# Kernel optimization log

Hardware: AMD Instinct MI355X
Metric: run time of the kernel (lower is better)

Reference implementation:

```python
import jax, jax.numpy as jnp
import numpy as np
from jax import lax

C_LIGHT = 3e8
SPATIAL, CROP = 64, 128
BIN_LEN, WALL, SAMP_COEFF, CYCLES = 0.01, 2.0, 2.0, 5
B, D = 2, 1


def _waveconvparam(bin_resolution, virtual_wavelength, cycles):
    samples = int(round(cycles * virtual_wavelength / (C_LIGHT * bin_resolution)))
    num_cycles = samples * (C_LIGHT * bin_resolution) / virtual_wavelength
    sigma = 0.3
    g = np.arange(samples, dtype=np.float64)
    env = np.exp(-(((g - samples / 2.0) / (samples / 2.0)) ** 2) / (2 * sigma ** 2))
    cos_k = np.cos(2 * np.pi * num_cycles * g / samples) * env
    sin_k = np.sin(2 * np.pi * num_cycles * g / samples) * env
    return cos_k, sin_k


def _define_psf(N, M, slope):
    # LCT psf: locus of min |(4 slope)^2 (x^2+y^2) - z|, normalized and circularly shifted
    x = np.arange(2 * N, dtype=np.float64) / (2 * N - 1) * 2 - 1
    z = np.arange(2 * M, dtype=np.float64) / (2 * M - 1) * 2
    gy, gx, gz = np.meshgrid(x, x, z)  # (2N,2N,2M)
    blur = np.abs((4 * slope) ** 2 * (gx ** 2 + gy ** 2) - gz)
    d = (np.abs(blur - blur.min(axis=2, keepdims=True)) < 1e-8).astype(np.float64)
    e = d / np.sqrt(d.sum())
    f = np.roll(np.roll(e, N, axis=0), N, axis=1)
    return np.transpose(f, (2, 0, 1))  # (2M,2N,2N)


def _resampling_operator(M):
    row = M * M
    x = np.arange(1, row + 1, dtype=np.float64)
    mtx = np.zeros((row, M), dtype=np.float64)
    mtx[np.arange(row), np.ceil(np.sqrt(x)).astype(np.int64) - 1] = 1.0
    mtx = mtx / np.sqrt(x)[:, None]
    mtxi = mtx.T.copy()
    for _ in range(int(np.log2(M))):
        mtx = 0.5 * (mtx[0::2] + mtx[1::2])
        mtxi = 0.5 * (mtxi[:, 0::2] + mtxi[:, 1::2])
    return mtx.astype(np.float32), mtxi.astype(np.float32)


def setup_inputs() -> dict:
    key = jax.random.key(0)
    kf, kw, kb = jax.random.split(key, 3)
    bin_res = BIN_LEN / C_LIGHT
    trange = CROP * C_LIGHT * bin_res
    slope = (WALL / 2.0) / trange
    vlam = SAMP_COEFF * 2.0 * (WALL / (SPATIAL - 1))
    cos_k, sin_k = _waveconvparam(bin_res, vlam, CYCLES)
    wave = np.stack([cos_k, sin_k], 0)[:, ::-1][:, None, :].astype(np.float32)  # (2,1,k)
    psf = _define_psf(SPATIAL, CROP, slope)
    invpsf = np.conj(np.fft.fftn(psf))
    mtx, mtxi = _resampling_operator(CROP)
    return {
        "feature": jax.random.normal(kf, (B, D, CROP, SPATIAL, SPATIAL), jnp.float32),
        "conv_w": jax.random.normal(kw, ()) * 0.1 + 1.0,
        "conv_b": jax.random.normal(kb, ()) * 0.1,
        "wave": jnp.asarray(wave),
        "invpsf_real": jnp.asarray(np.real(invpsf).astype(np.float32))[None],
        "invpsf_imag": jnp.asarray(np.imag(invpsf).astype(np.float32))[None],
        "mtx": jnp.asarray(mtx),
        "mtxi": jnp.asarray(mtxi),
    }


def _attention(k1, k2, w, b):
    # SE-style cross attention; Conv3d(1,1,1) on unbatched (C=1,T,H,W) is w*x+b
    T = k2.shape[1]
    pe = jnp.sin(jnp.arange(T, dtype=k2.dtype))  # PE3D with 1 channel -> sin along T
    k2p = k2 + pe[None, :, None, None]
    scal = jnp.mean(w * k1 + b)  # conv + adaptive_avg_pool3d(1), channel dim = 1
    q = (w * k2p + b).reshape(1, 1, -1)
    attn = jax.nn.sigmoid(jax.nn.softmax(scal * q, axis=2)).reshape(k2p.shape)
    return attn * k2p


def _fre_atten2(kernel, w, b):
    _, T, H, W = kernel.shape
    ct, ch, cw = T // 2, H // 2, W // 2
    st, sh, sw = (T - ct) // 2, (H - ch) // 2, (W - cw) // 2
    sl = (slice(None), slice(ct - st, ct + st), slice(ch - sh, ch + sh), slice(cw - sw, cw + sw))
    high = kernel[sl]
    low = jnp.roll(kernel, (ct, ch, cw), axis=(1, 2, 3))[sl]
    l2l = _attention(low, low, w, b)
    l2h = _attention(l2l, high, w, b)
    temp = kernel.at[sl].set(l2h)
    temp = jnp.roll(temp, (ct, ch, cw), axis=(1, 2, 3)).at[sl].set(l2l)
    return jnp.roll(temp, (ct, ch, cw), axis=(1, 2, 3))


def _forward(feature, conv_w, conv_b, wave, invpsf_real, invpsf_imag, mtx, mtxi):
    b, d, T, H, W = feature.shape
    BD = b * d
    k = wave.shape[2]
    # virtual wave conv along time: (BDHW,1,T) x (2,1,k)
    data = feature.reshape(BD, T, H, W).transpose(0, 2, 3, 1).reshape(-1, 1, T)
    conv = lax.conv_general_dilated(data, wave, (1,), [(k // 2, k // 2)],
                                    dimension_numbers=("NCH", "OIH", "NCH"))
    if k % 2 == 0:
        conv = conv[:, :, 1:]
    data2 = conv.reshape(BD, H, W, 2, T).transpose(3, 0, 4, 1, 2).reshape(2 * BD, T, H, W)
    # temporal resampling then zero-pad to 2T,2H,2W
    tmp = jnp.einsum("tm,bmx->btx", mtx, data2.reshape(2 * BD, T, H * W)).reshape(2 * BD, T, H, W)
    datapad = jnp.zeros((2 * BD, 2 * T, 2 * H, 2 * W), feature.dtype).at[:, :T, :H, :W].set(tmp)
    datafre = jnp.fft.fftn(datapad)  # torch.fft.fftn transforms ALL dims incl. batch
    w1 = _fre_atten2(invpsf_real, conv_w, conv_b)
    w2 = _fre_atten2(invpsf_imag, conv_w, conv_b)
    re_real = datafre.real * w1 - datafre.imag * w2
    re_imag = datafre.real * w2 + datafre.imag * w1
    re = jnp.fft.ifftn(lax.complex(re_real, re_imag))
    vol = re[:, :T, :H, :W]
    cr, ci = vol[:BD].real, vol[:BD].imag
    sr, si = vol[BD:].real, vol[BD:].imag
    sum_real = cr ** 2 - ci ** 2 + sr ** 2 - si ** 2
    sum_imag = 2 * cr * ci + 2 * sr * si
    mag = jax.nn.relu((jnp.sqrt(sum_real ** 2 + sum_imag ** 2) + sum_real) * 0.5)
    sq = jnp.sqrt(mag)
    out = jnp.einsum("tm,bmx->btx", mtxi, sq.reshape(BD, T, H * W))
    return out.reshape(b, d, T, H, W)


def reference(feature, conv_w, conv_b, wave, invpsf_real, invpsf_imag, mtx, mtxi):
    return _forward(feature, conv_w, conv_b, wave, invpsf_real, invpsf_imag, mtx, mtxi)
```

## Files before the change

kernel.cpp:

```cpp
#include <hip/hip_runtime.h>

#define BLKE 524288
#define VOLE 4194304
#define TCROP 2097152
#define PI2 6.283185307179586476925286766559

__device__ __forceinline__ float2 cmulf(float2 a, float2 b){
  return make_float2(a.x*b.x - a.y*b.y, a.x*b.y + a.y*b.x);
}
__device__ __forceinline__ float waveSum(float v){
  #pragma unroll
  for (int o=32;o;o>>=1) v += __shfl_xor(v,o);
  return v;
}
__device__ __forceinline__ float waveMaxf(float v){
  #pragma unroll
  for (int o=32;o;o>>=1) v = fmaxf(v,__shfl_xor(v,o));
  return v;
}
__device__ __forceinline__ float waveMinf(float v){
  #pragma unroll
  for (int o=32;o;o>>=1) v = fminf(v,__shfl_xor(v,o));
  return v;
}

__device__ __forceinline__ void bcastReduce5(const float* __restrict__ pA, int kap,
    float& sum, float& mnl, float& mxl, float& mnh, float& mxh, float* sm ){
  int tid = threadIdx.x;
  const float* q = pA + kap*1280 + tid*5;
  float s = q[0], a = q[1], b = q[2], c = q[3], d = q[4];
  s = waveSum(s); a = waveMinf(a); b = waveMaxf(b); c = waveMinf(c); d = waveMaxf(d);
  if ((tid&63)==0){ int w = tid>>6; sm[w]=s; sm[4+w]=a; sm[8+w]=b; sm[12+w]=c; sm[16+w]=d; }
  __syncthreads();
  sum = sm[0]+sm[1]+sm[2]+sm[3];
  mnl = fminf(fminf(sm[4],sm[5]),fminf(sm[6],sm[7]));
  mxl = fmaxf(fmaxf(sm[8],sm[9]),fmaxf(sm[10],sm[11]));
  mnh = fminf(fminf(sm[12],sm[13]),fminf(sm[14],sm[15]));
  mxh = fmaxf(fmaxf(sm[16],sm[17]),fmaxf(sm[18],sm[19]));
}

__device__ __forceinline__ float bcastSum256(const float* __restrict__ p, float* sm ){
  int tid = threadIdx.x;
  float s = waveSum(p[tid]);
  if ((tid&63)==0) sm[tid>>6] = s;
  __syncthreads();
  return sm[0]+sm[1]+sm[2]+sm[3];
}

__global__ void __launch_bounds__(256) kD1(const float* __restrict__ mtx,
                                           const float* __restrict__ wave,
                                           float* __restrict__ M,
                                           const float* __restrict__ Kr,
                                           const float* __restrict__ Ki,
                                           float* __restrict__ Lw, float* __restrict__ Hw,
                                           float* __restrict__ pA,
                                           float2* __restrict__ twF,
                                           float2* __restrict__ twD,
                                           float2* __restrict__ twI){
  __shared__ float spe[128];
  __shared__ float sm[20];
  int bid = blockIdx.x;
  int tid = threadIdx.x;
  if (bid < 512){
    int kap = bid >> 8, bx = bid & 255;
    const float* K = kap ? Ki : Kr;
    if (tid < 128) spe[tid] = sinf((float)tid);
    __syncthreads();
    float sum=0.f, mnl=3.4e38f, mxl=-3.4e38f, mnh=3.4e38f, mxh=-3.4e38f;
    int base = bx*256 + tid;
    #pragma unroll
    for (int it = 0; it < 8; it++){
      int e = base + it*65536;
      int tau = e >> 12, rem = e & 4095, eta = rem >> 6, om = rem & 63;
      float pe = spe[tau];
      float lo = K[(size_t)((tau+192)&255)*16384 + ((eta+96)&127)*128 + ((om+96)&127)];
      float hi = K[(size_t)(tau+64)*16384 + (eta+32)*128 + (om+32)];
      sum += lo;
      float lp = lo+pe, hp = hi+pe;
      Lw[kap*BLKE + e] = lp;
      Hw[kap*BLKE + e] = hp;
      mnl=fminf(mnl,lp); mxl=fmaxf(mxl,lp);
      mnh=fminf(mnh,hp); mxh=fmaxf(mxh,hp);
    }
    sum = waveSum(sum); mnl=waveMinf(mnl); mxl=waveMaxf(mxl); mnh=waveMinf(mnh); mxh=waveMaxf(mxh);
    if ((tid&63)==0){ int w=tid>>6; sm[w]=sum; sm[4+w]=mnl; sm[8+w]=mxl; sm[12+w]=mnh; sm[16+w]=mxh; }
    __syncthreads();
    if (tid==0){
      float* o = pA + kap*1280 + bx*5;
      o[0] = sm[0]+sm[1]+sm[2]+sm[3];
      o[1] = fminf(fminf(sm[4],sm[5]),fminf(sm[6],sm[7]));
      o[2] = fmaxf(fmaxf(sm[8],sm[9]),fmaxf(sm[10],sm[11]));
      o[3] = fminf(fminf(sm[12],sm[13]),fminf(sm[14],sm[15]));
      o[4] = fmaxf(fmaxf(sm[16],sm[17]),fmaxf(sm[18],sm[19]));
    }
  } else if (bid < 640){
    int idx = (bid-512)*256 + tid;
    int o = idx >> 14, r = idx & 16383;
    int t = r >> 7, s = r & 127;
    float acc = 0.f;
    int mlo = s-31; if (mlo < 0) mlo = 0;
    int mhi = s+31; if (mhi > 127) mhi = 127;
    for (int m = mlo; m <= mhi; m++) acc += mtx[t*128+m]*wave[o*63 + (s-m+31)];
    M[idx] = acc;
  } else {
    if (tid < 256){
      double ang = -PI2 * (double)tid / 256.0;
      twF[tid] = make_float2((float)cos(ang), (float)sin(ang));
    }
    if (tid < 64){
      double a2 = -PI2 * (double)tid / 128.0;
      twD[tid] = make_float2((float)cos(a2), (float)sin(a2));
      double a3 =  PI2 * (double)tid / 128.0;
      twI[tid] = make_float2((float)cos(a3), (float)sin(a3));
    }
  }
}

__global__ void __launch_bounds__(256) kD2(const float* __restrict__ feat,
                                           const float* __restrict__ M,
                                           float* __restrict__ tmp,
                                           const float* __restrict__ pA,
                                           const float* __restrict__ Lw,
                                           float* __restrict__ pB,
                                           const float* cw, const float* cb){
  __shared__ __align__(16) char smem[16640];
  __shared__ float sm[20], smo[4];
  int bid = blockIdx.x;
  int tid = threadIdx.x;
  if (bid < 512){
    int kap = bid >> 8, bx = bid & 255;
    float sum,mnl,mxl,mnh,mxh;
    bcastReduce5(pA,kap,sum,mnl,mxl,mnh,mxh,sm);
    float w = cw[0], b = cb[0];
    float s1 = w*(sum*(1.0f/BLKE)) + b;
    float a1 = s1*w, c1 = s1*b;
    float mx = (a1>=0.f) ? a1*mxl+c1 : a1*mnl+c1;
    float acc = 0.f;
    int base = kap*BLKE + bx*256 + tid;
    #pragma unroll
    for (int it = 0; it < 8; it++){
      float lp = Lw[base + it*65536];
      acc += expf(a1*lp + c1 - mx);
    }
    acc = waveSum(acc);
    if ((tid&63)==0) smo[tid>>6] = acc;
    __syncthreads();
    if (tid==0) pB[kap*256 + bx] = smo[0]+smo[1]+smo[2]+smo[3];
  } else {
    int e = bid - 512;
    int b = e >> 8, tt = (e >> 6) & 3, xt = e & 63;
    float (*LF)[64] = (float(*)[64])smem;
    float (*LM)[32][33] = (float(*)[32][33])(smem + 8192);
    int xx = tid & 63, tq = tid >> 6;
    float acc0[8] = {}, acc1[8] = {};
    const float* fb = feat + (size_t)b*BLKE;
    for (int sb = 0; sb < 4; sb++){
      #pragma unroll
      for (int j = 0; j < 8; j++){
        int idx = tid + j*256; int s = idx >> 6, x = idx & 63;
        LF[s][x] = fb[(size_t)(sb*32+s)*4096 + xt*64 + x];
      }
      #pragma unroll
      for (int j = 0; j < 8; j++){
        int idx = tid + j*256; int o = idx >> 10, r = idx & 1023;
        int trow = r >> 5, s = r & 31;
        LM[o][trow][s] = M[o*16384 + (tt*32+trow)*128 + sb*32+s];
      }
      __syncthreads();
      for (int s = 0; s < 32; s++){
        float f = LF[s][xx];
        #pragma unroll
        for (int i = 0; i < 8; i++){
          acc0[i] += LM[0][tq*8+i][s]*f;
          acc1[i] += LM[1][tq*8+i][s]*f;
        }
      }
      __syncthreads();
    }
    #pragma unroll
    for (int i = 0; i < 8; i++){
      int t = tt*32 + tq*8 + i;
      tmp[(size_t)(0*2+b)*BLKE + (size_t)t*4096 + xt*64+xx] = acc0[i];
      tmp[(size_t)(1*2+b)*BLKE + (size_t)t*4096 + xt*64+xx] = acc1[i];
    }
  }
}

__global__ void __launch_bounds__(256) kD3(const float* __restrict__ tmp,
                                           float2* __restrict__ Z2,
                                           const float* __restrict__ pA,
                                           const float* __restrict__ pB,
                                           const float* __restrict__ Lw,
                                           float* __restrict__ pC,
                                           const float* cw, const float* cb,
                                           const float2* __restrict__ twg){
  __shared__ __align__(16) char smem[8832];
  __shared__ float sm[20], smB[4], smo[4];
  int bid = blockIdx.x;
  int tid = threadIdx.x;
  if (bid < 512){
    int kap = bid >> 8, bx = bid & 255;
    float sum,mnl,mxl,mnh,mxh;
    bcastReduce5(pA,kap,sum,mnl,mxl,mnh,mxh,sm);
    float d1 = bcastSum256(pB + kap*256, smB);
    float w = cw[0], b = cb[0];
    float s1 = w*(sum*(1.0f/BLKE)) + b;
    float a1 = s1*w, c1 = s1*b;
    float mx = (a1>=0.f) ? a1*mxl+c1 : a1*mnl+c1;
    float invd = 1.0f/d1;
    float acc = 0.f;
    int base = kap*BLKE + bx*256 + tid;
    #pragma unroll
    for (int it = 0; it < 8; it++){
      float lp = Lw[base + it*65536];
      float p = expf(a1*lp + c1 - mx)*invd;
      acc += lp/(1.f + expf(-p));
    }
    acc = waveSum(acc);
    if ((tid&63)==0) smo[tid>>6] = acc;
    __syncthreads();
    if (tid==0) pC[kap*256 + bx] = smo[0]+smo[1]+smo[2]+smo[3];
  } else {
    int e = bid - 512;
    int b = e >> 11, bx = e & 2047;
    float2 (*bA)[130] = (float2(*)[130])smem;
    float2 (*bB)[130] = (float2(*)[130])(smem + 4160);
    float2* tw = (float2*)(smem + 8320);
    if (tid < 64) tw[tid] = twg[tid];
    int l = tid >> 6, lane = tid & 63;
    int line = bx*4 + l;
    int t = line >> 6, h = line & 63;
    const float* pc = tmp + (size_t)b*BLKE + (size_t)t*4096 + h*64;
    const float* ps = tmp + (size_t)(2+b)*BLKE + (size_t)t*4096 + h*64;
    bA[l][lane] = make_float2(pc[lane], ps[lane]);
    bA[l][lane+64] = make_float2(0.f, 0.f);
    __syncthreads();
    float2 (*src)[130] = bA, (*dst)[130] = bB;
    int m = 1;
    #pragma unroll
    for (int st = 0; st < 7; st++){
      int i = lane;
      int jm = i & ~(m-1);
      float2 a = src[l][i], b2 = src[l][i+64];
      float2 s = make_float2(a.x+b2.x, a.y+b2.y);
      float2 d = make_float2(a.x-b2.x, a.y-b2.y);
      dst[l][i+jm]   = s;
      dst[l][i+jm+m] = cmulf(d, tw[jm]);
      __syncthreads();
      float2 (*tp)[130] = src; src = dst; dst = tp;
      m <<= 1;
    }
    float2* outp = Z2 + (size_t)b*TCROP + (size_t)t*16384 + (size_t)h*128;
    outp[lane]    = src[l][lane];
    outp[lane+64] = src[l][lane+64];
  }
}

__global__ void __launch_bounds__(256) kD4(float2* __restrict__ Z2,
                                           const float* __restrict__ pA,
                                           const float* __restrict__ pC,
                                           const float* __restrict__ Hw,
                                           float* __restrict__ pD,
                                           const float* cw, const float* cb,
                                           const float2* __restrict__ twg){
  __shared__ __align__(16) char smem[33792];
  __shared__ float sm[20], smC[4], smo[4];
  int bid = blockIdx.x;
  int tid = threadIdx.x;
  if (bid < 512){
    int kap = bid >> 8, bx = bid & 255;
    float sum,mnl,mxl,mnh,mxh;
    bcastReduce5(pA,kap,sum,mnl,mxl,mnh,mxh,sm);
    float sl2 = bcastSum256(pC + kap*256, smC);
    float w = cw[0], b = cb[0];
    float s2 = w*(sl2*(1.0f/BLKE)) + b;
    float a2 = s2*w, c2 = s2*b;
    float mx = (a2>=0.f) ? a2*mxh+c2 : a2*mnh+c2;
    float acc = 0.f;
    int base = kap*BLKE + bx*256 + tid;
    #pragma unroll
    for (int it = 0; it < 8; it++){
      float hp = Hw[base + it*65536];
      acc += expf(a2*hp + c2 - mx);
    }
    acc = waveSum(acc);
    if ((tid&63)==0) smo[tid>>6] = acc;
    __syncthreads();
    if (tid==0) pD[kap*256 + bx] = smo[0]+smo[1]+smo[2]+smo[3];
  } else {
    int e = bid - 512;
    int b = e >> 10, bx = e & 1023;
    float2 (*bA)[130] = (float2(*)[130])smem;
    float2 (*bB)[130] = (float2(*)[130])(smem + 16640);
    float2* tw = (float2*)(smem + 33280);
    if (tid < 64) tw[tid] = twg[tid];
    float2* Z = Z2 + (size_t)b*TCROP;
    int t = bx >> 3; int w0 = (bx & 7) << 4;
    size_t base = (size_t)t*16384 + w0;
    #pragma unroll
    for (int q = 0; q < 4; q++){
      int idx = q*256 + tid; int wl = idx & 15, hh = idx >> 4;
      bA[wl][hh] = Z[base + (size_t)hh*128 + wl];
      bA[wl][hh+64] = make_float2(0.f, 0.f);
    }
    __syncthreads();
    float2 (*src)[130] = bA, (*dst)[130] = bB;
    int m = 1;
    #pragma unroll
    for (int st = 0; st < 7; st++){
      #pragma unroll
      for (int q = 0; q < 4; q++){
        int g = q*256 + tid; int li = g >> 6; int i = g & 63;
        int jm = i & ~(m-1);
        float2 a = src[li][i], b2 = src[li][i+64];
        float2 s = make_float2(a.x+b2.x, a.y+b2.y);
        float2 d = make_float2(a.x-b2.x, a.y-b2.y);
        dst[li][i+jm]   = s;
        dst[li][i+jm+m] = cmulf(d, tw[jm]);
      }
      __syncthreads();
      float2 (*tp)[130] = src; src = dst; dst = tp;
      m <<= 1;
    }
    #pragma unroll
    for (int q = 0; q < 8; q++){
      int idx = q*256 + tid; int wl = idx & 15, hh = idx >> 4;
      Z[base + (size_t)hh*128 + wl] = src[wl][hh];
    }
  }
}

__device__ __forceinline__ float attnv(float v, float a, float c, float mx, float invd){
  float p = expf(a*v + c - mx)*invd;
  return v / (1.f + expf(-p));
}
__device__ __forceinline__ float2 wcAt(int t, int h, int w,
                                       const float* __restrict__ Kr, const float* __restrict__ Ki,
                                       const float* spe, const float* P){
  size_t off = (size_t)t*16384 + (size_t)h*128 + w;
  float kr = Kr[off], ki = Ki[off];
  bool center = (t>=64 && t<192) && (h>=32 && h<96) && (w>=32 && w<96);
  int tc = (t+64)&255, hc = (h+32)&127, wc = (w+32)&127;
  bool corner = (tc<128) && (hc<64) && (wc<64);
  bool act = center || corner;
  float pe = spe[(center ? (t-64) : tc) & 127];
  float A0 = center?P[4]:P[0],   C0 = center?P[5]:P[1];
  float M0 = center?P[6]:P[2],   I0 = center?P[7]:P[3];
  float A1 = center?P[12]:P[8],  C1 = center?P[13]:P[9];
  float M1 = center?P[14]:P[10], I1 = center?P[15]:P[11];
  float ox = attnv(kr+pe, A0, C0, M0, I0);
  float oy = attnv(ki+pe, A1, C1, M1, I1);
  return make_float2(act?ox:kr, act?oy:ki);
}

__global__ void __launch_bounds__(256) kP(const float* __restrict__ pA,
                                          const float* __restrict__ pB,
                                          const float* __restrict__ pC,
                                          const float* __restrict__ pD,
                                          const float* cw, const float* cb,
                                          float* __restrict__ Pg){
  __shared__ float sm[20], smB[4], smC[4], smD[4];
  int tid = threadIdx.x;
  for (int kap = 0; kap < 2; kap++){
    if (kap) __syncthreads();
    float sum,mnl,mxl,mnh,mxh;
    bcastReduce5(pA,kap,sum,mnl,mxl,mnh,mxh,sm);
    float d1  = bcastSum256(pB + kap*256, smB);
    float sl2 = bcastSum256(pC + kap*256, smC);
    float d2  = bcastSum256(pD + kap*256, smD);
    if (tid==0){
      float w = cw[0], b = cb[0];
      float s1 = w*(sum*(1.0f/BLKE)) + b;
      float a1 = s1*w, c1 = s1*b;
      float mx1 = (a1>=0.f) ? a1*mxl+c1 : a1*mnl+c1;
      float s2 = w*(sl2*(1.0f/BLKE)) + b;
      float a2 = s2*w, c2 = s2*b;
      float mx2 = (a2>=0.f) ? a2*mxh+c2 : a2*mnh+c2;
      float* Q = Pg + kap*8;
      Q[0]=a1; Q[1]=c1; Q[2]=mx1; Q[3]=1.0f/d1;
      Q[4]=a2; Q[5]=c2; Q[6]=mx2; Q[7]=1.0f/d2;
    }
  }
}

__global__ void __launch_bounds__(256) kWc(const float* __restrict__ Kr,
                                           const float* __restrict__ Ki,
                                           const float* __restrict__ Pg,
                                           float2* __restrict__ Wc){
  __shared__ float spe[128];
  __shared__ float P[16];
  int tid = threadIdx.x;
  if (tid < 128) spe[tid] = sinf((float)tid);
  else if (tid < 144) P[tid-128] = Pg[tid-128];
  __syncthreads();
  #pragma unroll
  for (int q = 0; q < 4; q++){
    int idx = blockIdx.x*1024 + q*256 + tid;
    int t = idx >> 14, r = idx & 16383, h = r >> 7, w = r & 127;
    Wc[idx] = wcAt(t, h, w, Kr, Ki, spe, P);
  }
}

__global__ void __launch_bounds__(512) kTfused(const float2* __restrict__ Z2,
                                               float2* __restrict__ U2,
                                               float2* __restrict__ V2,
                                               const float2* __restrict__ Wc,
                                               const float2* __restrict__ twg){
  __shared__ float2 buf[16][259];
  __shared__ float2 tw[256];
  int tid = threadIdx.x;
  if (tid < 256) tw[tid] = twg[tid];
  int b = blockIdx.y;
  int bid = blockIdx.x;
  int h = bid >> 3, w0 = (bid & 7) << 4;
  int wl = tid & 15, pq = tid >> 4;
  const float2* Z = Z2 + (size_t)b*TCROP;
  size_t gbase = (size_t)h*128 + w0 + wl;
  #pragma unroll
  for (int q = 0; q < 4; q++){
    int p = q*32 + pq;
    buf[wl][p] = Z[(size_t)p*16384 + gbase];
    buf[wl][p+128] = make_float2(0.f, 0.f);
  }
  __syncthreads();
  #pragma unroll
  for (int st = 0; st < 4; st++){
    const int Q = 64 >> (2*st);
    const int f = 1 << (2*st);
    #pragma unroll
    for (int it = 0; it < 2; it++){
      int u = pq + 32*it;
      int j = u & (Q-1);
      int seg = u >> (6 - 2*st);
      int base = (seg << (8 - 2*st)) + j;
      float2 a0 = buf[wl][base];
      float2 a1 = buf[wl][base+Q];
      float2 a2 = buf[wl][base+2*Q];
      float2 a3 = buf[wl][base+3*Q];
      float2 t0 = make_float2(a0.x+a2.x, a0.y+a2.y);
      float2 t1 = make_float2(a0.x-a2.x, a0.y-a2.y);
      float2 t2 = make_float2(a1.x+a3.x, a1.y+a3.y);
      float2 t3 = make_float2(a1.x-a3.x, a1.y-a3.y);
      float2 z0 = make_float2(t0.x+t2.x, t0.y+t2.y);
      float2 z2 = make_float2(t0.x-t2.x, t0.y-t2.y);
      float2 z1 = make_float2(t1.x+t3.y, t1.y-t3.x);
      float2 z3 = make_float2(t1.x-t3.y, t1.y+t3.x);
      buf[wl][base]     = z0;
      buf[wl][base+Q]   = cmulf(z1, tw[f*j]);
      buf[wl][base+2*Q] = cmulf(z2, tw[2*f*j]);
      buf[wl][base+3*Q] = cmulf(z3, tw[3*f*j]);
    }
    __syncthreads();
  }
  float2 rg[8];
  #pragma unroll
  for (int q = 0; q < 8; q++) rg[q] = buf[wl][q*32 + pq];
  #pragma unroll
  for (int q = 0; q < 8; q++){
    int p = q*32 + pq;
    int kt = ((p&3)<<6) | (((p>>2)&3)<<4) | (((p>>4)&3)<<2) | ((p>>6)&3);
    float2 wc = Wc[(size_t)kt*16384 + (size_t)h*128 + w0 + wl];
    buf[wl][p] = cmulf(rg[q], wc);
  }
  __syncthreads();
  #pragma unroll
  for (int st = 0; st < 4; st++){
    const int Q = 1 << (2*st);
    const int f = 64 >> (2*st);
    #pragma unroll
    for (int it = 0; it < 2; it++){
      int u = pq + 32*it;
      int j = u & (Q-1);
      int seg = u >> (2*st);
      int base = (seg << (2*st + 2)) + j;
      float2 w1 = tw[f*j], w2 = tw[2*f*j], w3 = tw[3*f*j];
      float2 a0 = buf[wl][base];
      float2 r1 = buf[wl][base+Q];
      float2 r2 = buf[wl][base+2*Q];
      float2 r3 = buf[wl][base+3*Q];
      float2 b1 = make_float2(r1.x*w1.x + r1.y*w1.y, r1.y*w1.x - r1.x*w1.y);
      float2 b2 = make_float2(r2.x*w2.x + r2.y*w2.y, r2.y*w2.x - r2.x*w2.y);
      float2 b3 = make_float2(r3.x*w3.x + r3.y*w3.y, r3.y*w3.x - r3.x*w3.y);
      float2 t0 = make_float2(a0.x+b2.x, a0.y+b2.y);
      float2 t1 = make_float2(a0.x-b2.x, a0.y-b2.y);
      float2 t2 = make_float2(b1.x+b3.x, b1.y+b3.y);
      float2 t3 = make_float2(b1.x-b3.x, b1.y-b3.y);
      buf[wl][base]     = make_float2(t0.x+t2.x, t0.y+t2.y);
      buf[wl][base+Q]   = make_float2(t1.x-t3.y, t1.y+t3.x);
      buf[wl][base+2*Q] = make_float2(t0.x-t2.x, t0.y-t2.y);
      buf[wl][base+3*Q] = make_float2(t1.x+t3.y, t1.y-t3.x);
    }
    __syncthreads();
  }
  float2* Uo = U2 + (size_t)b*TCROP;
  #pragma unroll
  for (int q = 0; q < 4; q++){
    int p = q*32 + pq;
    Uo[(size_t)p*16384 + gbase] = buf[wl][p];
  }
  #pragma unroll
  for (int q = 0; q < 8; q++){
    int p = q*32 + pq;
    int kt = ((p&3)<<6) | (((p>>2)&3)<<4) | (((p>>4)&3)<<2) | ((p>>6)&3);
    int tm = (256-kt)&255, hm = (128-h)&127, wm = (128-(w0+wl))&127;
    float2 wc = Wc[(size_t)tm*16384 + (size_t)hm*128 + wm];
    wc.y = -wc.y;
    buf[wl][p] = cmulf(rg[q], wc);
  }
  __syncthreads();
  #pragma unroll
  for (int st = 0; st < 4; st++){
    const int Q = 1 << (2*st);
    const int f = 64 >> (2*st);
    #pragma unroll
    for (int it = 0; it < 2; it++){
      int u = pq + 32*it;
      int j = u & (Q-1);
      int seg = u >> (2*st);
      int base = (seg << (2*st + 2)) + j;
      float2 w1 = tw[f*j], w2 = tw[2*f*j], w3 = tw[3*f*j];
      float2 a0 = buf[wl][base];
      float2 r1 = buf[wl][base+Q];
      float2 r2 = buf[wl][base+2*Q];
      float2 r3 = buf[wl][base+3*Q];
      float2 b1 = make_float2(r1.x*w1.x + r1.y*w1.y, r1.y*w1.x - r1.x*w1.y);
      float2 b2 = make_float2(r2.x*w2.x + r2.y*w2.y, r2.y*w2.x - r2.x*w2.y);
      float2 b3 = make_float2(r3.x*w3.x + r3.y*w3.y, r3.y*w3.x - r3.x*w3.y);
      float2 t0 = make_float2(a0.x+b2.x, a0.y+b2.y);
      float2 t1 = make_float2(a0.x-b2.x, a0.y-b2.y);
      float2 t2 = make_float2(b1.x+b3.x, b1.y+b3.y);
      float2 t3 = make_float2(b1.x-b3.x, b1.y-b3.y);
      buf[wl][base]     = make_float2(t0.x+t2.x, t0.y+t2.y);
      buf[wl][base+Q]   = make_float2(t1.x-t3.y, t1.y+t3.x);
      buf[wl][base+2*Q] = make_float2(t0.x-t2.x, t0.y-t2.y);
      buf[wl][base+3*Q] = make_float2(t1.x+t3.y, t1.y-t3.x);
    }
    __syncthreads();
  }
  float2* Vo = V2 + (size_t)b*TCROP;
  #pragma unroll
  for (int q = 0; q < 4; q++){
    int p = q*32 + pq;
    Vo[(size_t)p*16384 + gbase] = buf[wl][p];
  }
}

__global__ void __launch_bounds__(1024) kHW(const float2* __restrict__ U2,
                                            const float2* __restrict__ V2,
                                            float* __restrict__ sq,
                                            const float2* __restrict__ twg){
  __shared__ float2 plane[16384];
  __shared__ float2 tw[64];
  int tid = threadIdx.x;
  if (tid < 64) tw[tid] = twg[tid];
  int t = blockIdx.x, b = blockIdx.y;
  size_t off = (size_t)b*TCROP + (size_t)t*16384;
  float2 yr[4];
  #pragma unroll
  for (int uv = 0; uv < 2; uv++){
    const float2* src = (uv ? V2 : U2) + off;
    #pragma unroll
    for (int it = 0; it < 16; it++){
      int idx = it*1024 + tid;
      plane[idx] = src[idx];
    }
    __syncthreads();
    float4* P4 = (float4*)plane;
    #pragma unroll
    for (int s = 6; s >= 0; s--){
      int m = 1 << s, sh = 6 - s;
      #pragma unroll
      for (int it = 0; it < 4; it++){
        int task = it*1024 + tid;
        int w2 = task & 63, pr = task >> 6;
        int j = pr & (m-1);
        int pos = ((pr & ~(m-1)) << 1) | j;
        float4 a  = P4[pos*64 + w2];
        float4 bq = P4[(pos+m)*64 + w2];
        float2 twv = tw[j << sh];
        float4 sv;
        sv.x = a.x+bq.x; sv.y = a.y+bq.y; sv.z = a.z+bq.z; sv.w = a.w+bq.w;
        float dx = a.x-bq.x, dy = a.y-bq.y, dz = a.z-bq.z, dw = a.w-bq.w;
        float4 dv;
        dv.x = dx*twv.x - dy*twv.y; dv.y = dx*twv.y + dy*twv.x;
        dv.z = dz*twv.x - dw*twv.y; dv.w = dz*twv.y + dw*twv.x;
        P4[pos*64 + w2]     = sv;
        P4[(pos+m)*64 + w2] = dv;
      }
      __syncthreads();
    }
    #pragma unroll
    for (int s = 6; s >= 0; s--){
      int m = 1 << s, sh = 6 - s;
      #pragma unroll
      for (int it = 0; it < 4; it++){
        int task = it*1024 + tid;
        int pr = task & 63;
        int hr = (task >> 6) << 1;
        int j = pr & (m-1);
        int pos = ((pr & ~(m-1)) << 1) | j;
        float2 a  = plane[hr*128 + pos];
        float2 bq = plane[hr*128 + pos + m];
        float2 twv = tw[j << sh];
        float2 d = make_float2(a.x-bq.x, a.y-bq.y);
        plane[hr*128 + pos]     = make_float2(a.x+bq.x, a.y+bq.y);
        plane[hr*128 + pos + m] = cmulf(d, twv);
      }
      __syncthreads();
    }
    #pragma unroll
    for (int it = 0; it < 4; it++){
      int oidx = it*1024 + tid;
      int h = oidx >> 6, w = oidx & 63;
      int hr = (int)(__brev((unsigned)h) >> 25);
      int wr = (int)(__brev((unsigned)w) >> 25);
      float2 v = plane[hr*128 + wr];
      if (uv == 0){
        yr[it] = v;
      } else {
        float2 y = yr[it];
        const float sc = 1.0f/(float)VOLE;
        const float sc2 = sc*sc;
        float2 sv = cmulf(y, make_float2(v.x, -v.y));
        sv.x *= sc2; sv.y *= sc2;
        float mag = 0.5f*(sqrtf(sv.x*sv.x + sv.y*sv.y) + sv.x);
        mag = fmaxf(mag, 0.f);
        sq[(size_t)b*BLKE + (size_t)t*4096 + oidx] = sqrtf(mag);
      }
    }
    if (uv == 0) __syncthreads();
  }
}

__global__ void __launch_bounds__(256) kOut(const float* __restrict__ sq,
                                            const float* __restrict__ mtxi,
                                            float* __restrict__ out){
  __shared__ float LF[32][64];
  __shared__ float LM[32][33];
  int b = blockIdx.z, tt = blockIdx.y, xt = blockIdx.x;
  int tid = threadIdx.x;
  int xx = tid & 63, tq = tid >> 6;
  float acc[8] = {};
  const float* fb = sq + (size_t)b*BLKE;
  for (int sb = 0; sb < 4; sb++){
    #pragma unroll
    for (int j = 0; j < 8; j++){
      int idx = tid + j*256; int s = idx >> 6, x = idx & 63;
      LF[s][x] = fb[(size_t)(sb*32+s)*4096 + xt*64 + x];
    }
    #pragma unroll
    for (int j = 0; j < 4; j++){
      int idx = tid + j*256; int trow = idx >> 5, s = idx & 31;
      LM[trow][s] = mtxi[(tt*32+trow)*128 + sb*32+s];
    }
    __syncthreads();
    for (int s = 0; s < 32; s++){
      float f = LF[s][xx];
      #pragma unroll
      for (int i = 0; i < 8; i++) acc[i] += LM[tq*8+i][s]*f;
    }
    __syncthreads();
  }
  #pragma unroll
  for (int i = 0; i < 8; i++){
    int t = tt*32 + tq*8 + i;
    out[(size_t)b*BLKE + (size_t)t*4096 + xt*64+xx] = acc[i];
  }
}

extern "C" void kernel_launch(void* const* d_in, const int* in_sizes, int n_in,
                              void* d_out, int out_size, void* d_ws, size_t ws_size,
                              hipStream_t stream){
  const float* feature = (const float*)d_in[0];
  const float* convW   = (const float*)d_in[1];
  const float* convB   = (const float*)d_in[2];
  const float* wave    = (const float*)d_in[3];
  const float* Kr      = (const float*)d_in[4];
  const float* Ki      = (const float*)d_in[5];
  const float* mtx     = (const float*)d_in[6];
  const float* mtxi    = (const float*)d_in[7];
  float* out = (float*)d_out;
  float* ws  = (float*)d_ws;

  float*  M    = ws;
  float*  pA   = ws + 32832;
  float*  pB   = ws + 35392;
  float*  pC   = ws + 35904;
  float*  pD   = ws + 36416;
  float*  Pg   = ws + 37440;
  float2* twF  = (float2*)(ws + 40960);
  float2* twD  = (float2*)(ws + 41472);
  float2* twI  = (float2*)(ws + 41600);
  float*  tmp  = ws + 65536;
  float*  sq   = ws + 65536 + 2097152;
  float2* Z2   = (float2*)(ws + 3211264);
  float2* U2   = (float2*)(ws + 11599872);
  float2* V2   = (float2*)(ws + 19988480);
  float2* Wc   = (float2*)(ws + 28377088);
  float*  Lw   = (float*)U2;
  float*  Hw   = ((float*)U2) + 1048576;

  kD1 <<<641,  256, 0, stream>>>(mtx, wave, M, Kr, Ki, Lw, Hw, pA, twF, twD, twI);
  kD2 <<<1024, 256, 0, stream>>>(feature, M, tmp, pA, Lw, pB, convW, convB);
  kD3 <<<4608, 256, 0, stream>>>(tmp, Z2, pA, pB, Lw, pC, convW, convB, twD);
  kD4 <<<2560, 256, 0, stream>>>(Z2, pA, pC, Hw, pD, convW, convB, twD);
  kP  <<<1,    256, 0, stream>>>(pA, pB, pC, pD, convW, convB, Pg);
  kWc <<<4096, 256, 0, stream>>>(Kr, Ki, Pg, Wc);
  kTfused<<<dim3(1024,2), 512, 0, stream>>>(Z2, U2, V2, Wc, twF);
  kHW<<<dim3(128,2), 1024, 0, stream>>>(U2, V2, sq, twI);
  kOut<<<dim3(64,4,2), 256, 0, stream>>>(sq, mtxi, out);
}
```

Before: 268.0 us.

## Fuse W and H forward FFTs into one shared-memory 2D plane kernel

The W-axis FFT that used to sit inside kD3 and the H-axis FFT that used to sit inside kD4 now run in a single new kernel, kFwd. It loads each zero-padded 128x128 plane into 128 KB of LDS in bit-reversed order and does both radix-2 passes in place, the second pass using float4 accesses. The attention reductions are split out into small standalone kernels. This removes the round trip of Z2 through global memory between the two 1D FFT passes. In exchange, occupancy drops to one 1024-thread block per CU with a large LDS footprint, and only 256 blocks are launched.

After: 268.3 us. About the same (+0.1%).

```diff
diff --git a/kernel.cpp b/kernel.cpp
--- a/kernel.cpp
+++ b/kernel.cpp
@@ -186,148 +186,64 @@
   }
 }
 
-__global__ void __launch_bounds__(256) kD3(const float* __restrict__ tmp,
-                                           float2* __restrict__ Z2,
-                                           const float* __restrict__ pA,
-                                           const float* __restrict__ pB,
-                                           const float* __restrict__ Lw,
-                                           float* __restrict__ pC,
-                                           const float* cw, const float* cb,
-                                           const float2* __restrict__ twg){
-  __shared__ __align__(16) char smem[8832];
+__global__ void __launch_bounds__(256) kD3a(const float* __restrict__ pA,
+                                            const float* __restrict__ pB,
+                                            const float* __restrict__ Lw,
+                                            float* __restrict__ pC,
+                                            const float* cw, const float* cb){
   __shared__ float sm[20], smB[4], smo[4];
   int bid = blockIdx.x;
   int tid = threadIdx.x;
-  if (bid < 512){
-    int kap = bid >> 8, bx = bid & 255;
-    float sum,mnl,mxl,mnh,mxh;
-    bcastReduce5(pA,kap,sum,mnl,mxl,mnh,mxh,sm);
-    float d1 = bcastSum256(pB + kap*256, smB);
-    float w = cw[0], b = cb[0];
-    float s1 = w*(sum*(1.0f/BLKE)) + b;
-    float a1 = s1*w, c1 = s1*b;
-    float mx = (a1>=0.f) ? a1*mxl+c1 : a1*mnl+c1;
-    float invd = 1.0f/d1;
-    float acc = 0.f;
-    int base = kap*BLKE + bx*256 + tid;
-    #pragma unroll
-    for (int it = 0; it < 8; it++){
-      float lp = Lw[base + it*65536];
-      float p = expf(a1*lp + c1 - mx)*invd;
-      acc += lp/(1.f + expf(-p));
-    }
-    acc = waveSum(acc);
-    if ((tid&63)==0) smo[tid>>6] = acc;
-    __syncthreads();
-    if (tid==0) pC[kap*256 + bx] = smo[0]+smo[1]+smo[2]+smo[3];
-  } else {
-    int e = bid - 512;
-    int b = e >> 11, bx = e & 2047;
-    float2 (*bA)[130] = (float2(*)[130])smem;
-    float2 (*bB)[130] = (float2(*)[130])(smem + 4160);
-    float2* tw = (float2*)(smem + 8320);
-    if (tid < 64) tw[tid] = twg[tid];
-    int l = tid >> 6, lane = tid & 63;
-    int line = bx*4 + l;
-    int t = line >> 6, h = line & 63;
-    const float* pc = tmp + (size_t)b*BLKE + (size_t)t*4096 + h*64;
-    const float* ps = tmp + (size_t)(2+b)*BLKE + (size_t)t*4096 + h*64;
-    bA[l][lane] = make_float2(pc[lane], ps[lane]);
-    bA[l][lane+64] = make_float2(0.f, 0.f);
-    __syncthreads();
-    float2 (*src)[130] = bA, (*dst)[130] = bB;
-    int m = 1;
-    #pragma unroll
-    for (int st = 0; st < 7; st++){
-      int i = lane;
-      int jm = i & ~(m-1);
-      float2 a = src[l][i], b2 = src[l][i+64];
-      float2 s = make_float2(a.x+b2.x, a.y+b2.y);
-      float2 d = make_float2(a.x-b2.x, a.y-b2.y);
-      dst[l][i+jm]   = s;
-      dst[l][i+jm+m] = cmulf(d, tw[jm]);
-      __syncthreads();
-      float2 (*tp)[130] = src; src = dst; dst = tp;
-      m <<= 1;
-    }
-    float2* outp = Z2 + (size_t)b*TCROP + (size_t)t*16384 + (size_t)h*128;
-    outp[lane]    = src[l][lane];
-    outp[lane+64] = src[l][lane+64];
-  }
-}
-
-__global__ void __launch_bounds__(256) kD4(float2* __restrict__ Z2,
-                                           const float* __restrict__ pA,
-                                           const float* __restrict__ pC,
-                                           const float* __restrict__ Hw,
-                                           float* __restrict__ pD,
-                                           const float* cw, const float* cb,
-                                           const float2* __restrict__ twg){
-  __shared__ __align__(16) char smem[33792];
+  int kap = bid >> 8, bx = bid & 255;
+  float sum,mnl,mxl,mnh,mxh;
+  bcastReduce5(pA,kap,sum,mnl,mxl,mnh,mxh,sm);
+  float d1 = bcastSum256(pB + kap*256, smB);
+  float w = cw[0], b = cb[0];
+  float s1 = w*(sum*(1.0f/BLKE)) + b;
+  float a1 = s1*w, c1 = s1*b;
+  float mx = (a1>=0.f) ? a1*mxl+c1 : a1*mnl+c1;
+  float invd = 1.0f/d1;
+  float acc = 0.f;
+  int base = kap*BLKE + bx*256 + tid;
+  #pragma unroll
+  for (int it = 0; it < 8; it++){
+    float lp = Lw[base + it*65536];
+    float p = expf(a1*lp + c1 - mx)*invd;
+    acc += lp/(1.f + expf(-p));
+  }
+  acc = waveSum(acc);
+  if ((tid&63)==0) smo[tid>>6] = acc;
+  __syncthreads();
+  if (tid==0) pC[kap*256 + bx] = smo[0]+smo[1]+smo[2]+smo[3];
+}
+
+__global__ void __launch_bounds__(256) kD4a(const float* __restrict__ pA,
+                                            const float* __restrict__ pC,
+                                            const float* __restrict__ Hw,
+                                            float* __restrict__ pD,
+                                            const float* cw, const float* cb){
   __shared__ float sm[20], smC[4], smo[4];
   int bid = blockIdx.x;
   int tid = threadIdx.x;
-  if (bid < 512){
-    int kap = bid >> 8, bx = bid & 255;
-    float sum,mnl,mxl,mnh,mxh;
-    bcastReduce5(pA,kap,sum,mnl,mxl,mnh,mxh,sm);
-    float sl2 = bcastSum256(pC + kap*256, smC);
-    float w = cw[0], b = cb[0];
-    float s2 = w*(sl2*(1.0f/BLKE)) + b;
-    float a2 = s2*w, c2 = s2*b;
-    float mx = (a2>=0.f) ? a2*mxh+c2 : a2*mnh+c2;
-    float acc = 0.f;
-    int base = kap*BLKE + bx*256 + tid;
-    #pragma unroll
-    for (int it = 0; it < 8; it++){
-      float hp = Hw[base + it*65536];
-      acc += expf(a2*hp + c2 - mx);
-    }
-    acc = waveSum(acc);
-    if ((tid&63)==0) smo[tid>>6] = acc;
-    __syncthreads();
-    if (tid==0) pD[kap*256 + bx] = smo[0]+smo[1]+smo[2]+smo[3];
-  } else {
-    int e = bid - 512;
-    int b = e >> 10, bx = e & 1023;
-    float2 (*bA)[130] = (float2(*)[130])smem;
-    float2 (*bB)[130] = (float2(*)[130])(smem + 16640);
-    float2* tw = (float2*)(smem + 33280);
-    if (tid < 64) tw[tid] = twg[tid];
-    float2* Z = Z2 + (size_t)b*TCROP;
-    int t = bx >> 3; int w0 = (bx & 7) << 4;
-    size_t base = (size_t)t*16384 + w0;
-    #pragma unroll
-    for (int q = 0; q < 4; q++){
-      int idx = q*256 + tid; int wl = idx & 15, hh = idx >> 4;
-      bA[wl][hh] = Z[base + (size_t)hh*128 + wl];
-      bA[wl][hh+64] = make_float2(0.f, 0.f);
-    }
-    __syncthreads();
-    float2 (*src)[130] = bA, (*dst)[130] = bB;
-    int m = 1;
-    #pragma unroll
-    for (int st = 0; st < 7; st++){
-      #pragma unroll
-      for (int q = 0; q < 4; q++){
-        int g = q*256 + tid; int li = g >> 6; int i = g & 63;
-        int jm = i & ~(m-1);
-        float2 a = src[li][i], b2 = src[li][i+64];
-        float2 s = make_float2(a.x+b2.x, a.y+b2.y);
-        float2 d = make_float2(a.x-b2.x, a.y-b2.y);
-        dst[li][i+jm]   = s;
-        dst[li][i+jm+m] = cmulf(d, tw[jm]);
-      }
-      __syncthreads();
-      float2 (*tp)[130] = src; src = dst; dst = tp;
-      m <<= 1;
-    }
-    #pragma unroll
-    for (int q = 0; q < 8; q++){
-      int idx = q*256 + tid; int wl = idx & 15, hh = idx >> 4;
-      Z[base + (size_t)hh*128 + wl] = src[wl][hh];
-    }
-  }
+  int kap = bid >> 8, bx = bid & 255;
+  float sum,mnl,mxl,mnh,mxh;
+  bcastReduce5(pA,kap,sum,mnl,mxl,mnh,mxh,sm);
+  float sl2 = bcastSum256(pC + kap*256, smC);
+  float w = cw[0], b = cb[0];
+  float s2 = w*(sl2*(1.0f/BLKE)) + b;
+  float a2 = s2*w, c2 = s2*b;
+  float mx = (a2>=0.f) ? a2*mxh+c2 : a2*mnh+c2;
+  float acc = 0.f;
+  int base = kap*BLKE + bx*256 + tid;
+  #pragma unroll
+  for (int it = 0; it < 8; it++){
+    float hp = Hw[base + it*65536];
+    acc += expf(a2*hp + c2 - mx);
+  }
+  acc = waveSum(acc);
+  if ((tid&63)==0) smo[tid>>6] = acc;
+  __syncthreads();
+  if (tid==0) pD[kap*256 + bx] = smo[0]+smo[1]+smo[2]+smo[3];
 }
 
 __device__ __forceinline__ float attnv(float v, float a, float c, float mx, float invd){
@@ -398,6 +314,73 @@
     int idx = blockIdx.x*1024 + q*256 + tid;
     int t = idx >> 14, r = idx & 16383, h = r >> 7, w = r & 127;
     Wc[idx] = wcAt(t, h, w, Kr, Ki, spe, P);
+  }
+}
+
+__global__ void __launch_bounds__(1024) kFwd(const float* __restrict__ tmp,
+                                             float2* __restrict__ Z2,
+                                             const float2* __restrict__ twg){
+  __shared__ float2 plane[16384];
+  __shared__ float2 tw[64];
+  int tid = threadIdx.x;
+  if (tid < 64) tw[tid] = twg[tid];
+  int t = blockIdx.x, b = blockIdx.y;
+  #pragma unroll
+  for (int it = 0; it < 16; it++) plane[it*1024 + tid] = make_float2(0.f, 0.f);
+  __syncthreads();
+  const float* pc = tmp + (size_t)b*BLKE + (size_t)t*4096;
+  const float* ps = tmp + (size_t)(2+b)*BLKE + (size_t)t*4096;
+  #pragma unroll
+  for (int it = 0; it < 4; it++){
+    int idx = it*1024 + tid;
+    int h = idx >> 6, w = idx & 63;
+    int hr = (int)(__brev((unsigned)h) >> 25);
+    int wr = (int)(__brev((unsigned)w) >> 25);
+    plane[hr*128 + wr] = make_float2(pc[idx], ps[idx]);
+  }
+  __syncthreads();
+  #pragma unroll
+  for (int st = 0; st < 7; st++){
+    int m = 1 << st, sh = 6 - st;
+    #pragma unroll
+    for (int it = 0; it < 4; it++){
+      int task = it*1024 + tid;
+      int pr = task & 63;
+      int hr = (task >> 6) << 1;
+      int j = pr & (m-1);
+      int pos = ((pr & ~(m-1)) << 1) | j;
+      float2 a  = plane[hr*128 + pos];
+      float2 bq = cmulf(plane[hr*128 + pos + m], tw[j << sh]);
+      plane[hr*128 + pos]     = make_float2(a.x+bq.x, a.y+bq.y);
+      plane[hr*128 + pos + m] = make_float2(a.x-bq.x, a.y-bq.y);
+    }
+    __syncthreads();
+  }
+  float4* P4 = (float4*)plane;
+  #pragma unroll
+  for (int st = 0; st < 7; st++){
+    int m = 1 << st, sh = 6 - st;
+    #pragma unroll
+    for (int it = 0; it < 4; it++){
+      int task = it*1024 + tid;
+      int w2 = task & 63, pr = task >> 6;
+      int j = pr & (m-1);
+      int pos = ((pr & ~(m-1)) << 1) | j;
+      float4 a  = P4[pos*64 + w2];
+      float4 bq = P4[(pos+m)*64 + w2];
+      float2 twv = tw[j << sh];
+      float bx = bq.x*twv.x - bq.y*twv.y, by = bq.x*twv.y + bq.y*twv.x;
+      float bz = bq.z*twv.x - bq.w*twv.y, bw = bq.z*twv.y + bq.w*twv.x;
+      P4[pos*64 + w2]     = make_float4(a.x+bx, a.y+by, a.z+bz, a.w+bw);
+      P4[(pos+m)*64 + w2] = make_float4(a.x-bx, a.y-by, a.z-bz, a.w-bw);
+    }
+    __syncthreads();
+  }
+  float2* outp = Z2 + (size_t)b*TCROP + (size_t)t*16384;
+  #pragma unroll
+  for (int it = 0; it < 16; it++){
+    int idx = it*1024 + tid;
+    outp[idx] = plane[idx];
   }
 }
 
@@ -702,10 +685,11 @@
 
   kD1 <<<641,  256, 0, stream>>>(mtx, wave, M, Kr, Ki, Lw, Hw, pA, twF, twD, twI);
   kD2 <<<1024, 256, 0, stream>>>(feature, M, tmp, pA, Lw, pB, convW, convB);
-  kD3 <<<4608, 256, 0, stream>>>(tmp, Z2, pA, pB, Lw, pC, convW, convB, twD);
-  kD4 <<<2560, 256, 0, stream>>>(Z2, pA, pC, Hw, pD, convW, convB, twD);
+  kD3a<<<512,  256, 0, stream>>>(pA, pB, Lw, pC, convW, convB);
+  kD4a<<<512,  256, 0, stream>>>(pA, pC, Hw, pD, convW, convB);
   kP  <<<1,    256, 0, stream>>>(pA, pB, pC, pD, convW, convB, Pg);
   kWc <<<4096, 256, 0, stream>>>(Kr, Ki, Pg, Wc);
+  kFwd<<<dim3(128,2), 1024, 0, stream>>>(tmp, Z2, twD);
   kTfused<<<dim3(1024,2), 512, 0, stream>>>(Z2, U2, V2, Wc, twF);
   kHW<<<dim3(128,2), 1024, 0, stream>>>(U2, V2, sq, twI);
   kOut<<<dim3(64,4,2), 256, 0, stream>>>(sq, mtxi, out);
```
